# Optimization experiments

Measured on AMD Instinct MI355X. Metric: run time of the kernel, lower is better.

The kernel has to match this reference:

```python
import jax, jax.numpy as jnp
import numpy as np

N_DRUG, N_MICROBE = 1500, 1572
N = N_DRUG + N_MICROBE          # 3072 nodes
F_IN = 1546                     # raw feature dim (fc1: 1546 -> 256)
D0 = 256                        # GCN input dim after fc1
H1 = H2 = 128                   # GCN hidden dims (H1 + H2 = 256)
B = 16384                       # number of (left,right) query pairs


def _sym_norm(A):
    # D^{-1/2} A D^{-1/2} (no self loops), zeros kept for isolated nodes
    deg = A.sum(axis=1)
    d = jnp.where(deg > 0, jax.lax.rsqrt(deg), 0.0)
    return A * d[:, None] * d[None, :]


def _compute_inf(adj, L):
    # dl.compute_inf: L-hop influence = L-th power of sym-normalized adjacency
    An = _sym_norm(adj)
    M = An
    for _ in range(L - 1):
        M = M @ An
    return M


def _gcn_norm(W):
    # GCNConv normalization: add self loops (weight 1), sym-normalize by weighted degree
    Ahat = W + jnp.eye(W.shape[0], dtype=W.dtype)
    deg = Ahat.sum(axis=1)
    d = jnp.where(deg > 0, jax.lax.rsqrt(deg), 0.0)
    return Ahat * d[:, None] * d[None, :]


def _glorot(key, shape):
    return jax.random.normal(key, shape, dtype=jnp.float32) / np.sqrt(shape[0])


def setup_inputs() -> dict:
    key = jax.random.key(0)
    ks = jax.random.split(key, 24)
    u = jax.random.uniform(ks[0], (N, N), dtype=jnp.float32)
    w = jax.random.uniform(ks[1], (N, N), dtype=jnp.float32)
    adj = jnp.where(u < 0.01, w, 0.0)
    adj = jnp.maximum(adj, adj.T)
    X = jax.random.normal(ks[2], (N, F_IN), dtype=jnp.float32)
    left = jax.random.randint(ks[3], (B,), 0, N)
    right = jax.random.randint(ks[4], (B,), 0, N)
    return dict(
        left=left, right=right, X=X, adj=adj, threshold=jnp.float32(1e-4),
        W_fc1=_glorot(ks[5], (F_IN, D0)), b_fc1=jnp.zeros((D0,), jnp.float32),
        Wg1=_glorot(ks[6], (D0, H1)), bg1=jnp.zeros((H1,), jnp.float32),
        Wg2=_glorot(ks[7], (H1, H2)), bg2=jnp.zeros((H2,), jnp.float32),
        Wg3=_glorot(ks[8], (D0, H1)), bg3=jnp.zeros((H1,), jnp.float32),
        Wg4=_glorot(ks[9], (H1, H2)), bg4=jnp.zeros((H2,), jnp.float32),
        Wg5=_glorot(ks[10], (D0, H1)), bg5=jnp.zeros((H1,), jnp.float32),
        Wg6=_glorot(ks[11], (H1, H2)), bg6=jnp.zeros((H2,), jnp.float32),
        cnn_k=jax.random.normal(ks[12], (1, 3, 3, 3), dtype=jnp.float32) * 0.1,
        cnn_b=jnp.zeros((1,), jnp.float32),
        W_a=_glorot(ks[13], (2 * (H1 + H2), 64)), b_a=jnp.zeros((64,), jnp.float32),
        W_b=_glorot(ks[14], (64, 2)), b_b=jnp.zeros((2,), jnp.float32),
    )


def reference(left, right, X, adj, threshold,
              W_fc1, b_fc1, Wg1, bg1, Wg2, bg2, Wg3, bg3, Wg4, bg4,
              Wg5, bg5, Wg6, bg6, cnn_k, cnn_b, W_a, b_a, W_b, b_b):
    X0 = jax.nn.relu(X @ W_fc1 + b_fc1)  # fc1: [N, 1546] -> [N, 256]

    def branch(mask_src, Wa, ba, Wb, bb):
        # dynamically thresholded edges carry the ORIGINAL adj weights
        Wadj = jnp.where(mask_src > threshold, adj, 0.0)
        An = _gcn_norm(Wadj)                       # [N, N]
        e1 = jax.nn.relu(An @ (X0 @ Wa) + ba)      # GCNConv 1
        e2 = jax.nn.relu(An @ (e1 @ Wb) + bb)      # GCNConv 2
        return jnp.concatenate([e1, e2], axis=1)   # [N, 256]

    emb_l2 = branch(_compute_inf(adj, 2), Wg1, bg1, Wg2, bg2)
    emb_l1 = branch(_compute_inf(adj, 1), Wg3, bg3, Wg4, bg4)
    emb_l0 = branch(adj, Wg5, bg5, Wg6, bg6)

    emb = jnp.stack([emb_l0, emb_l1, emb_l2], axis=0)[None]  # [1, 3, N, 256]
    conv = jax.lax.conv_general_dilated(
        emb, cnn_k, window_strides=(1, 1), padding=[(2, 2), (2, 2)],
        rhs_dilation=(2, 2), dimension_numbers=('NCHW', 'OIHW', 'NCHW'))
    emb_all = conv[0, 0] + cnn_b[0]                # [N, 256]

    pair = jnp.concatenate([emb_all[left], emb_all[right]], axis=1)  # [B, 512]
    h = jax.nn.relu(pair @ W_a + b_a)              # dropout is identity at eval
    logits = h @ W_b + b_b                         # [B, 2]
    return logits, emb_all
```

## Files before the change

kernel.cpp:

```cpp
#include <hip/hip_runtime.h>

#define NN 3072
#define FIN 1546
#define KP 1568
#define MAXR 192
#define KSPLIT 7
#define KSLICE 224

typedef __attribute__((ext_vector_type(8))) __bf16 bf16x8;
typedef __attribute__((ext_vector_type(4))) float f32x4;

__global__ __launch_bounds__(256) void csr_k(const float* __restrict__ adj,
                                             int* __restrict__ cols, float* __restrict__ vals,
                                             int* __restrict__ cnt, float* __restrict__ dvec) {
    int i = blockIdx.x * 4 + (threadIdx.x >> 6);
    int lane = threadIdx.x & 63;
    const float* row = adj + (size_t)i * NN;
    float s = 0.f; int count = 0;
    int base = i * MAXR;
    for (int c = 0; c < NN; c += 64) {
        float a = row[c + lane];
        s += a;
        unsigned long long m = __ballot(a != 0.f);
        if (a != 0.f) {
            int pos = count + __popcll(m & ((1ull << lane) - 1ull));
            if (pos < MAXR) { cols[base + pos] = c + lane; vals[base + pos] = a; }
        }
        count += __popcll(m);
    }
    for (int off = 32; off; off >>= 1) s += __shfl_xor(s, off);
    if (lane == 0) {
        cnt[i] = count < MAXR ? count : MAXR;
        dvec[i] = (s > 0.f) ? 1.0f / sqrtf(s) : 0.f;
    }
}

__global__ void xsplit_k(const float* __restrict__ X, __bf16* __restrict__ Xh,
                         __bf16* __restrict__ Xl) {
    int idx = blockIdx.x * 256 + threadIdx.x;
    int i = idx / KP, c = idx - i * KP;
    float x = (c < FIN) ? X[(size_t)i * FIN + c] : 0.f;
    __bf16 h = (__bf16)x;
    Xh[idx] = h;
    Xl[idx] = (__bf16)(x - (float)h);
}

__global__ void wsplit_k(const float* __restrict__ W, __bf16* __restrict__ WhT,
                         __bf16* __restrict__ WlT) {
    int idx = blockIdx.x * 256 + threadIdx.x;
    int c = idx / KP, k = idx - c * KP;
    float x = (k < FIN) ? W[(size_t)k * 256 + c] : 0.f;
    __bf16 h = (__bf16)x;
    WhT[idx] = h;
    WlT[idx] = (__bf16)(x - (float)h);
}

__global__ __launch_bounds__(256) void fc1m_k(const __bf16* __restrict__ Xh,
                                              const __bf16* __restrict__ Xl,
                                              const __bf16* __restrict__ WhT,
                                              const __bf16* __restrict__ WlT,
                                              float* __restrict__ Cpart) {
    int tid = threadIdx.x;
    int w = tid >> 6, lane = tid & 63;
    int m = lane & 15, q = lane >> 4;
    int i0 = blockIdx.x * 64, c0 = blockIdx.y * 64;
    int z = blockIdx.z;
    int k0 = z * KSLICE;
    int rowA = i0 + w * 16 + m;
    const __bf16* xh = Xh + (size_t)rowA * KP + k0 + q * 8;
    const __bf16* xl = Xl + (size_t)rowA * KP + k0 + q * 8;
    const __bf16* bh0 = WhT + (size_t)(c0 + m) * KP + k0 + q * 8;
    const __bf16* bl0 = WlT + (size_t)(c0 + m) * KP + k0 + q * 8;

    f32x4 acc[4];
    #pragma unroll
    for (int ct = 0; ct < 4; ct++)
        #pragma unroll
        for (int r = 0; r < 4; r++) acc[ct][r] = 0.f;

    for (int ks = 0; ks < KSLICE; ks += 32) {
        bf16x8 ah = *(const bf16x8*)(xh + ks);
        bf16x8 al = *(const bf16x8*)(xl + ks);
        #pragma unroll
        for (int ct = 0; ct < 4; ct++) {
            bf16x8 bh = *(const bf16x8*)(bh0 + (size_t)ct * 16 * KP + ks);
            bf16x8 bl = *(const bf16x8*)(bl0 + (size_t)ct * 16 * KP + ks);
            acc[ct] = __builtin_amdgcn_mfma_f32_16x16x32_bf16(ah, bh, acc[ct], 0, 0, 0);
            acc[ct] = __builtin_amdgcn_mfma_f32_16x16x32_bf16(ah, bl, acc[ct], 0, 0, 0);
            acc[ct] = __builtin_amdgcn_mfma_f32_16x16x32_bf16(al, bh, acc[ct], 0, 0, 0);
        }
    }
    float* outp = Cpart + (size_t)z * NN * 256;
    int rowBase = i0 + w * 16 + q * 4;
    #pragma unroll
    for (int ct = 0; ct < 4; ct++) {
        int col = c0 + ct * 16 + m;
        #pragma unroll
        for (int r = 0; r < 4; r++)
            outp[(size_t)(rowBase + r) * 256 + col] = acc[ct][r];
    }
}

__global__ void reduce7_k(const float* __restrict__ Cpart, const float* __restrict__ bias,
                          float* __restrict__ X0) {
    int idx4 = blockIdx.x * 256 + threadIdx.x;
    int c4 = (idx4 & 63) << 2;
    float4 s = ((const float4*)Cpart)[idx4];
    #pragma unroll
    for (int z = 1; z < KSPLIT; z++) {
        float4 t = ((const float4*)(Cpart + (size_t)z * NN * 256))[idx4];
        s.x += t.x; s.y += t.y; s.z += t.z; s.w += t.w;
    }
    float4 b = *(const float4*)&bias[c4];
    s.x = fmaxf(s.x + b.x, 0.f); s.y = fmaxf(s.y + b.y, 0.f);
    s.z = fmaxf(s.z + b.z, 0.f); s.w = fmaxf(s.w + b.w, 0.f);
    ((float4*)X0)[idx4] = s;
}

__global__ __launch_bounds__(256) void maskall_k(const int* __restrict__ cols,
                                                 const float* __restrict__ vals,
                                                 const int* __restrict__ cnt,
                                                 const float* __restrict__ dvec,
                                                 const float* __restrict__ thrp,
                                                 int* __restrict__ mcols,
                                                 float* __restrict__ mvals,
                                                 int* __restrict__ mcnt,
                                                 float* __restrict__ db) {
    __shared__ float ds[NN];
    __shared__ int lcols[MAXR];
    __shared__ float lvals[MAXR];
    __shared__ int lcnt;
    __shared__ float osum;
    int i = blockIdx.x, tid = threadIdx.x, mode = blockIdx.y;
    mcols += (size_t)mode * NN * MAXR;
    mvals += (size_t)mode * NN * MAXR;
    mcnt  += (size_t)mode * NN;
    db    += (size_t)mode * NN;
    int ni = cnt[i], base = i * MAXR;
    float thr = *thrp;
    float di = dvec[i];

    if (mode < 2) {
        if (tid == 0) lcnt = 0;
        __syncthreads();
        float s = 0.f;
        if (tid < ni) {
            int j = cols[base + tid];
            float a = vals[base + tid];
            float m = (mode == 0) ? a : a * di * dvec[j];
            if (m > thr) {
                int p = atomicAdd(&lcnt, 1);
                mcols[base + p] = j;
                mvals[base + p] = a;
                s = a;
            }
        }
        ds[tid] = s; __syncthreads();
        for (int off = 128; off; off >>= 1) {
            if (tid < off) ds[tid] += ds[tid + off];
            __syncthreads();
        }
        if (tid == 0) {
            mcnt[i] = lcnt;
            db[i] = 1.0f / sqrtf(ds[0] + 1.0f);
        }
        return;
    }

    if (tid == 0) { osum = 0.f; lcnt = 0; }
    for (int j = tid; j < NN; j += 256) ds[j] = 0.f;
    __syncthreads();
    for (int t = tid; t < ni; t += 256) {
        int j = cols[base + t];
        float a = vals[base + t];
        lcols[t] = j; lvals[t] = a;
        ds[j] = a * dvec[j] * dvec[j];
    }
    __syncthreads();
    int lane = tid & 63, wv = tid >> 6;
    int sub = lane & 15, dg = lane >> 4;
    for (int o = wv * 4 + dg; o < ni; o += 16) {
        int j = lcols[o];
        int nj = cnt[j], bj = j * MAXR;
        float dot = 0.f;
        for (int t = sub; t < nj; t += 16)
            dot += vals[bj + t] * ds[cols[bj + t]];
        #pragma unroll
        for (int off = 8; off; off >>= 1) dot += __shfl_xor(dot, off);
        if (sub == 0 && di * dvec[j] * dot > thr) {
            int p = atomicAdd(&lcnt, 1);
            mcols[base + p] = j;
            mvals[base + p] = lvals[o];
            atomicAdd(&osum, lvals[o]);
        }
    }
    __syncthreads();
    if (tid == 0) {
        mcnt[i] = lcnt;
        db[i] = 1.0f / sqrtf(osum + 1.0f);
    }
}

__global__ __launch_bounds__(256) void gemm3_k(const float* __restrict__ A, int aplane, int lda,
                                               const float* __restrict__ B0,
                                               const float* __restrict__ B1,
                                               const float* __restrict__ B2,
                                               int K, float* __restrict__ out) {
    __shared__ float Ast[16][68];
    __shared__ float Bs[16][64];
    int tid = threadIdx.x;
    int tx = tid & 15, ty = tid >> 4;
    int i0 = blockIdx.x * 64, c0 = blockIdx.y * 64;
    int z = blockIdx.z;
    const float* Ab = A + (size_t)z * aplane;
    const float* B = (z == 0) ? B0 : (z == 1) ? B1 : B2;
    float* outp = out + (size_t)z * NN * 128;
    int sr = tid >> 4, sk = tid & 15;
    int bk = tid >> 4, bc4 = (tid & 15) << 2;

    float ap[4]; float4 bp;
    #pragma unroll
    for (int u = 0; u < 4; u++) ap[u] = Ab[(size_t)(i0 + sr + u * 16) * lda + sk];
    bp = *(const float4*)&B[(size_t)bk * 128 + c0 + bc4];

    float acc[4][4];
    #pragma unroll
    for (int r = 0; r < 4; r++)
        #pragma unroll
        for (int c = 0; c < 4; c++) acc[r][c] = 0.f;

    for (int kt = 0; kt < K; kt += 16) {
        __syncthreads();
        #pragma unroll
        for (int u = 0; u < 4; u++) Ast[sk][sr + u * 16] = ap[u];
        *(float4*)&Bs[bk][bc4] = bp;
        __syncthreads();
        int kn = kt + 16;
        if (kn < K) {
            #pragma unroll
            for (int u = 0; u < 4; u++) ap[u] = Ab[(size_t)(i0 + sr + u * 16) * lda + kn + sk];
            bp = *(const float4*)&B[(size_t)(kn + bk) * 128 + c0 + bc4];
        }
        #pragma unroll
        for (int kk = 0; kk < 16; kk++) {
            float4 a = *(const float4*)&Ast[kk][ty * 4];
            float4 b = *(const float4*)&Bs[kk][tx * 4];
            const float* av = (const float*)&a;
            const float* bv = (const float*)&b;
            #pragma unroll
            for (int r = 0; r < 4; r++)
                #pragma unroll
                for (int c = 0; c < 4; c++) acc[r][c] += av[r] * bv[c];
        }
    }
    #pragma unroll
    for (int r = 0; r < 4; r++) {
        int row = i0 + ty * 4 + r;
        float4 v = make_float4(acc[r][0], acc[r][1], acc[r][2], acc[r][3]);
        *(float4*)&outp[(size_t)row * 128 + c0 + tx * 4] = v;
    }
}

__global__ __launch_bounds__(256) void spmm3_k(const int* __restrict__ mcols,
                                               const float* __restrict__ mvals,
                                               const int* __restrict__ mcnt,
                                               const float* __restrict__ db,
                                               const float* __restrict__ Xin,
                                               const float* __restrict__ bias0,
                                               const float* __restrict__ bias1,
                                               const float* __restrict__ bias2,
                                               float* __restrict__ outA,
                                               float* __restrict__ embf, int coff) {
    __shared__ float lcoef[MAXR];
    __shared__ int lj[MAXR];
    __shared__ float4 part[8][32];
    int i = blockIdx.x, tid = threadIdx.x, b = blockIdx.y;
    mcols += (size_t)b * NN * MAXR;
    mvals += (size_t)b * NN * MAXR;
    mcnt  += (size_t)b * NN;
    db    += (size_t)b * NN;
    const float* Xb = Xin + (size_t)b * NN * 128;
    const float* bias = (b == 0) ? bias0 : (b == 1) ? bias1 : bias2;
    float dbi = db[i];
    int n = mcnt[i], base = i * MAXR;
    if (tid < n) {
        int j = mcols[base + tid];
        lj[tid] = j;
        lcoef[tid] = mvals[base + tid] * dbi * db[j];
    }
    __syncthreads();
    int g = tid >> 5, c4 = (tid & 31) << 2;
    float4 acc = make_float4(0.f, 0.f, 0.f, 0.f);
    if (g == 0) {
        float4 x = *(const float4*)&Xb[(size_t)i * 128 + c4];
        float d2 = dbi * dbi;
        acc = make_float4(d2 * x.x, d2 * x.y, d2 * x.z, d2 * x.w);
    }
    for (int t = g; t < n; t += 8) {
        float cf = lcoef[t];
        float4 x = *(const float4*)&Xb[(size_t)lj[t] * 128 + c4];
        acc.x += cf * x.x; acc.y += cf * x.y; acc.z += cf * x.z; acc.w += cf * x.w;
    }
    part[g][tid & 31] = acc;
    __syncthreads();
    if (tid < 32) {
        float4 s = part[0][tid];
        #pragma unroll
        for (int gg = 1; gg < 8; gg++) {
            float4 t4 = part[gg][tid];
            s.x += t4.x; s.y += t4.y; s.z += t4.z; s.w += t4.w;
        }
        int cc = tid << 2;
        float4 bv = *(const float4*)&bias[cc];
        s.x = fmaxf(s.x + bv.x, 0.f); s.y = fmaxf(s.y + bv.y, 0.f);
        s.z = fmaxf(s.z + bv.z, 0.f); s.w = fmaxf(s.w + bv.w, 0.f);
        if (outA) *(float4*)&outA[((size_t)b * NN + i) * 128 + cc] = s;
        *(float4*)&embf[((size_t)b * NN + i) * 256 + coff + cc] = s;
    }
}

__global__ __launch_bounds__(256) void conv3f_k(const float* __restrict__ emb,
                                                const float* __restrict__ ck,
                                                const float* __restrict__ cb,
                                                float* __restrict__ outf) {
    __shared__ float rows[3][3][256];
    int n = blockIdx.x, c = threadIdx.x;
    #pragma unroll
    for (int i = 0; i < 3; i++)
        #pragma unroll
        for (int kh = 0; kh < 3; kh++) {
            int nn2 = n + 2 * kh - 2;
            rows[i][kh][c] = (nn2 >= 0 && nn2 < NN) ? emb[((size_t)i * NN + nn2) * 256 + c] : 0.f;
        }
    __syncthreads();
    float s = cb[0];
    #pragma unroll
    for (int i = 0; i < 3; i++)
        #pragma unroll
        for (int kh = 0; kh < 3; kh++)
            #pragma unroll
            for (int kw = 0; kw < 3; kw++) {
                int cc = c + 2 * kw - 2;
                if (cc >= 0 && cc < 256)
                    s += rows[i][kh][cc] * ck[(i * 3 + kh) * 3 + kw];
            }
    outf[(size_t)n * 256 + c] = s;
}

__global__ __launch_bounds__(256) void gemmUV_k(const float* __restrict__ A,
                                                const float* __restrict__ Wa,
                                                float* __restrict__ uvp) {
    __shared__ float Ast[16][68];
    __shared__ float Bs[16][64];
    int tid = threadIdx.x;
    int tx = tid & 15, ty = tid >> 4;
    int i0 = blockIdx.x * 64;
    int half = blockIdx.y;
    int z = blockIdx.z;
    int ks = z * 128;
    const float* Bb = Wa + (half ? 256 * 64 : 0);
    int sr = tid >> 4, sk = tid & 15;
    int bk = tid >> 4, bc4 = (tid & 15) << 2;

    float ap[4]; float4 bp;
    #pragma unroll
    for (int u = 0; u < 4; u++) ap[u] = A[(size_t)(i0 + sr + u * 16) * 256 + ks + sk];
    bp = *(const float4*)&Bb[(size_t)(ks + bk) * 64 + bc4];

    float acc[4][4];
    #pragma unroll
    for (int r = 0; r < 4; r++)
        #pragma unroll
        for (int c = 0; c < 4; c++) acc[r][c] = 0.f;

    for (int kt = ks; kt < ks + 128; kt += 16) {
        __syncthreads();
        #pragma unroll
        for (int u = 0; u < 4; u++) Ast[sk][sr + u * 16] = ap[u];
        *(float4*)&Bs[bk][bc4] = bp;
        __syncthreads();
        int kn = kt + 16;
        if (kn < ks + 128) {
            #pragma unroll
            for (int u = 0; u < 4; u++) ap[u] = A[(size_t)(i0 + sr + u * 16) * 256 + kn + sk];
            bp = *(const float4*)&Bb[(size_t)(kn + bk) * 64 + bc4];
        }
        #pragma unroll
        for (int kk = 0; kk < 16; kk++) {
            float4 a = *(const float4*)&Ast[kk][ty * 4];
            float4 b = *(const float4*)&Bs[kk][tx * 4];
            const float* av = (const float*)&a;
            const float* bv = (const float*)&b;
            #pragma unroll
            for (int r = 0; r < 4; r++)
                #pragma unroll
                for (int c = 0; c < 4; c++) acc[r][c] += av[r] * bv[c];
        }
    }
    float* outp = uvp + (size_t)z * NN * 128;
    #pragma unroll
    for (int r = 0; r < 4; r++) {
        int row = i0 + ty * 4 + r;
        float4 v = make_float4(acc[r][0], acc[r][1], acc[r][2], acc[r][3]);
        *(float4*)&outp[(size_t)row * 128 + half * 64 + tx * 4] = v;
    }
}

__global__ __launch_bounds__(256) void pairuv_k(const int* __restrict__ left,
                                                const int* __restrict__ right,
                                                const float* __restrict__ uvp,
                                                const float* __restrict__ ba,
                                                const float* __restrict__ Wb,
                                                const float* __restrict__ bb,
                                                float* __restrict__ out) {
    int tid = threadIdx.x;
    int w = tid >> 6, c = tid & 63;
    int base = blockIdx.x * 16 + w * 4;
    const float* u0 = uvp;
    const float* u1 = uvp + (size_t)NN * 128;
    float bac = ba[c];
    float w0 = Wb[c * 2], w1 = Wb[c * 2 + 1];
    float b0 = bb[0], b1 = bb[1];
    #pragma unroll
    for (int pp = 0; pp < 4; pp++) {
        int row = base + pp;
        int l = left[row], r = right[row];
        float h = u0[(size_t)l * 128 + c] + u1[(size_t)l * 128 + c]
                + u0[(size_t)r * 128 + 64 + c] + u1[(size_t)r * 128 + 64 + c] + bac;
        h = fmaxf(h, 0.f);
        float s0 = h * w0, s1 = h * w1;
        for (int off = 32; off; off >>= 1) {
            s0 += __shfl_xor(s0, off);
            s1 += __shfl_xor(s1, off);
        }
        if (c == 0) {
            out[row * 2]     = s0 + b0;
            out[row * 2 + 1] = s1 + b1;
        }
    }
}

extern "C" void kernel_launch(void* const* d_in, const int* in_sizes, int n_in,
                              void* d_out, int out_size, void* d_ws, size_t ws_size,
                              hipStream_t stream) {
    const int* left  = (const int*)d_in[0];
    const int* right = (const int*)d_in[1];
    const float* X    = (const float*)d_in[2];
    const float* adj  = (const float*)d_in[3];
    const float* thr  = (const float*)d_in[4];
    const float* Wfc1 = (const float*)d_in[5];
    const float* bfc1 = (const float*)d_in[6];
    const float* Wga[3] = { (const float*)d_in[15], (const float*)d_in[11], (const float*)d_in[7] };
    const float* bga[3] = { (const float*)d_in[16], (const float*)d_in[12], (const float*)d_in[8] };
    const float* Wgb[3] = { (const float*)d_in[17], (const float*)d_in[13], (const float*)d_in[9] };
    const float* bgb[3] = { (const float*)d_in[18], (const float*)d_in[14], (const float*)d_in[10] };
    const float* cnnk = (const float*)d_in[19];
    const float* cnnb = (const float*)d_in[20];
    const float* Wa_  = (const float*)d_in[21];
    const float* ba_  = (const float*)d_in[22];
    const float* Wb_  = (const float*)d_in[23];
    const float* bb_  = (const float*)d_in[24];

    char* p = (char*)d_ws;
    auto take = [&](size_t n) { char* q = p; p += (n + 255) & ~(size_t)255; return q; };
    float* dvec = (float*)take(NN * 4);
    float* db3  = (float*)take((size_t)3 * NN * 4);
    int*   cnt  = (int*)take(NN * 4);
    int*   mcnt3 = (int*)take((size_t)3 * NN * 4);
    int*   cols = (int*)take((size_t)NN * MAXR * 4);
    float* vals = (float*)take((size_t)NN * MAXR * 4);
    int*   mcols3 = (int*)take((size_t)3 * NN * MAXR * 4);
    float* mvals3 = (float*)take((size_t)3 * NN * MAXR * 4);
    float* X0    = (float*)take((size_t)NN * 256 * 4);
    float* XWall = (float*)take((size_t)3 * NN * 128 * 4);
    float* e1all = (float*)take((size_t)3 * NN * 128 * 4);
    float* HW2all= (float*)take((size_t)3 * NN * 128 * 4);
    float* embf  = (float*)take((size_t)3 * NN * 256 * 4);
    __bf16* Xl   = (__bf16*)take((size_t)NN * KP * 2);
    __bf16* WhT  = (__bf16*)take((size_t)256 * KP * 2);
    __bf16* WlT  = (__bf16*)take((size_t)256 * KP * 2);
    __bf16* Xh = (__bf16*)mcols3;
    float* Cpart = XWall;
    float* uvp = embf;

    float* out_logits = (float*)d_out;
    float* out_emb = out_logits + 32768;

    csr_k<<<NN / 4, 256, 0, stream>>>(adj, cols, vals, cnt, dvec);
    xsplit_k<<<NN * KP / 256, 256, 0, stream>>>(X, Xh, Xl);
    wsplit_k<<<256 * KP / 256, 256, 0, stream>>>(Wfc1, WhT, WlT);
    fc1m_k<<<dim3(NN / 64, 4, KSPLIT), 256, 0, stream>>>(Xh, Xl, WhT, WlT, Cpart);
    reduce7_k<<<NN * 64 / 256, 256, 0, stream>>>(Cpart, bfc1, X0);

    maskall_k<<<dim3(NN, 3), 256, 0, stream>>>(cols, vals, cnt, dvec, thr,
                                               mcols3, mvals3, mcnt3, db3);

    gemm3_k<<<dim3(NN / 64, 2, 3), 256, 0, stream>>>(X0, 0, 256, Wga[0], Wga[1], Wga[2], 256, XWall);
    spmm3_k<<<dim3(NN, 3), 256, 0, stream>>>(mcols3, mvals3, mcnt3, db3, XWall,
                                             bga[0], bga[1], bga[2], e1all, embf, 0);
    gemm3_k<<<dim3(NN / 64, 2, 3), 256, 0, stream>>>(e1all, NN * 128, 128, Wgb[0], Wgb[1], Wgb[2], 128, HW2all);
    spmm3_k<<<dim3(NN, 3), 256, 0, stream>>>(mcols3, mvals3, mcnt3, db3, HW2all,
                                             bgb[0], bgb[1], bgb[2], (float*)0, embf, 128);

    conv3f_k<<<NN, 256, 0, stream>>>(embf, cnnk, cnnb, out_emb);
    gemmUV_k<<<dim3(NN / 64, 2, 2), 256, 0, stream>>>(out_emb, Wa_, uvp);
    pairuv_k<<<16384 / 16, 256, 0, stream>>>(left, right, uvp, ba_, Wb_, bb_, out_logits);
}
```

Baseline: 325.2 us.

## Fuse prep kernels and drop split-K in fc1 GEMM with fused bias-ReLU

Merges the CSR build, X split and W split kernels into one launch that dispatches on block index, cutting two launches. The fc1 GEMM drops its 7-way K split and the separate reduction kernel. Each block now has 2 waves covering 32 rows and walks the full K, applying bias and ReLU in the epilogue, so the partial-sum write and re-read go away. The cost is fewer, longer blocks: 384 blocks of 128 threads, each with a serial K loop of 49 steps. That may lower latency hiding compared with the 1344 split-K blocks used before.

```diff
diff --git a/kernel.cpp b/kernel.cpp
--- a/kernel.cpp
+++ b/kernel.cpp
@@ -4,16 +4,43 @@
 #define FIN 1546
 #define KP 1568
 #define MAXR 192
-#define KSPLIT 7
-#define KSLICE 224
+
+#define XSPLIT_BLOCKS (NN * KP / 256)
+#define WSPLIT_BLOCKS (256 * KP / 256)
+#define CSR_BLOCKS (NN / 4)
 
 typedef __attribute__((ext_vector_type(8))) __bf16 bf16x8;
 typedef __attribute__((ext_vector_type(4))) float f32x4;
 
-__global__ __launch_bounds__(256) void csr_k(const float* __restrict__ adj,
-                                             int* __restrict__ cols, float* __restrict__ vals,
-                                             int* __restrict__ cnt, float* __restrict__ dvec) {
-    int i = blockIdx.x * 4 + (threadIdx.x >> 6);
+__global__ __launch_bounds__(256) void prep_k(const float* __restrict__ adj,
+                                              int* __restrict__ cols, float* __restrict__ vals,
+                                              int* __restrict__ cnt, float* __restrict__ dvec,
+                                              const float* __restrict__ X,
+                                              __bf16* __restrict__ Xh, __bf16* __restrict__ Xl,
+                                              const float* __restrict__ W,
+                                              __bf16* __restrict__ WhT, __bf16* __restrict__ WlT) {
+    int bid = blockIdx.x;
+    if (bid < XSPLIT_BLOCKS) {
+        int idx = bid * 256 + threadIdx.x;
+        int i = idx / KP, c = idx - i * KP;
+        float x = (c < FIN) ? X[(size_t)i * FIN + c] : 0.f;
+        __bf16 h = (__bf16)x;
+        Xh[idx] = h;
+        Xl[idx] = (__bf16)(x - (float)h);
+        return;
+    }
+    bid -= XSPLIT_BLOCKS;
+    if (bid < WSPLIT_BLOCKS) {
+        int idx = bid * 256 + threadIdx.x;
+        int c = idx / KP, k = idx - c * KP;
+        float x = (k < FIN) ? W[(size_t)k * 256 + c] : 0.f;
+        __bf16 h = (__bf16)x;
+        WhT[idx] = h;
+        WlT[idx] = (__bf16)(x - (float)h);
+        return;
+    }
+    bid -= WSPLIT_BLOCKS;
+    int i = bid * 4 + (threadIdx.x >> 6);
     int lane = threadIdx.x & 63;
     const float* row = adj + (size_t)i * NN;
     float s = 0.f; int count = 0;
@@ -35,42 +62,21 @@
     }
 }
 
-__global__ void xsplit_k(const float* __restrict__ X, __bf16* __restrict__ Xh,
-                         __bf16* __restrict__ Xl) {
-    int idx = blockIdx.x * 256 + threadIdx.x;
-    int i = idx / KP, c = idx - i * KP;
-    float x = (c < FIN) ? X[(size_t)i * FIN + c] : 0.f;
-    __bf16 h = (__bf16)x;
-    Xh[idx] = h;
-    Xl[idx] = (__bf16)(x - (float)h);
-}
-
-__global__ void wsplit_k(const float* __restrict__ W, __bf16* __restrict__ WhT,
-                         __bf16* __restrict__ WlT) {
-    int idx = blockIdx.x * 256 + threadIdx.x;
-    int c = idx / KP, k = idx - c * KP;
-    float x = (k < FIN) ? W[(size_t)k * 256 + c] : 0.f;
-    __bf16 h = (__bf16)x;
-    WhT[idx] = h;
-    WlT[idx] = (__bf16)(x - (float)h);
-}
-
-__global__ __launch_bounds__(256) void fc1m_k(const __bf16* __restrict__ Xh,
+__global__ __launch_bounds__(128) void fc1m_k(const __bf16* __restrict__ Xh,
                                               const __bf16* __restrict__ Xl,
                                               const __bf16* __restrict__ WhT,
                                               const __bf16* __restrict__ WlT,
-                                              float* __restrict__ Cpart) {
+                                              const float* __restrict__ bias,
+                                              float* __restrict__ X0) {
     int tid = threadIdx.x;
     int w = tid >> 6, lane = tid & 63;
     int m = lane & 15, q = lane >> 4;
-    int i0 = blockIdx.x * 64, c0 = blockIdx.y * 64;
-    int z = blockIdx.z;
-    int k0 = z * KSLICE;
+    int i0 = blockIdx.x * 32, c0 = blockIdx.y * 64;
     int rowA = i0 + w * 16 + m;
-    const __bf16* xh = Xh + (size_t)rowA * KP + k0 + q * 8;
-    const __bf16* xl = Xl + (size_t)rowA * KP + k0 + q * 8;
-    const __bf16* bh0 = WhT + (size_t)(c0 + m) * KP + k0 + q * 8;
-    const __bf16* bl0 = WlT + (size_t)(c0 + m) * KP + k0 + q * 8;
+    const __bf16* xh = Xh + (size_t)rowA * KP + q * 8;
+    const __bf16* xl = Xl + (size_t)rowA * KP + q * 8;
+    const __bf16* bh0 = WhT + (size_t)(c0 + m) * KP + q * 8;
+    const __bf16* bl0 = WlT + (size_t)(c0 + m) * KP + q * 8;
 
     f32x4 acc[4];
     #pragma unroll
@@ -78,7 +84,7 @@
         #pragma unroll
         for (int r = 0; r < 4; r++) acc[ct][r] = 0.f;
 
-    for (int ks = 0; ks < KSLICE; ks += 32) {
+    for (int ks = 0; ks < KP; ks += 32) {
         bf16x8 ah = *(const bf16x8*)(xh + ks);
         bf16x8 al = *(const bf16x8*)(xl + ks);
         #pragma unroll
@@ -90,31 +96,15 @@
             acc[ct] = __builtin_amdgcn_mfma_f32_16x16x32_bf16(al, bh, acc[ct], 0, 0, 0);
         }
     }
-    float* outp = Cpart + (size_t)z * NN * 256;
     int rowBase = i0 + w * 16 + q * 4;
     #pragma unroll
     for (int ct = 0; ct < 4; ct++) {
         int col = c0 + ct * 16 + m;
+        float bc = bias[col];
         #pragma unroll
         for (int r = 0; r < 4; r++)
-            outp[(size_t)(rowBase + r) * 256 + col] = acc[ct][r];
-    }
-}
-
-__global__ void reduce7_k(const float* __restrict__ Cpart, const float* __restrict__ bias,
-                          float* __restrict__ X0) {
-    int idx4 = blockIdx.x * 256 + threadIdx.x;
-    int c4 = (idx4 & 63) << 2;
-    float4 s = ((const float4*)Cpart)[idx4];
-    #pragma unroll
-    for (int z = 1; z < KSPLIT; z++) {
-        float4 t = ((const float4*)(Cpart + (size_t)z * NN * 256))[idx4];
-        s.x += t.x; s.y += t.y; s.z += t.z; s.w += t.w;
-    }
-    float4 b = *(const float4*)&bias[c4];
-    s.x = fmaxf(s.x + b.x, 0.f); s.y = fmaxf(s.y + b.y, 0.f);
-    s.z = fmaxf(s.z + b.z, 0.f); s.w = fmaxf(s.w + b.w, 0.f);
-    ((float4*)X0)[idx4] = s;
+            X0[(size_t)(rowBase + r) * 256 + col] = fmaxf(acc[ct][r] + bc, 0.f);
+    }
 }
 
 __global__ __launch_bounds__(256) void maskall_k(const int* __restrict__ cols,
@@ -480,17 +470,15 @@
     __bf16* WhT  = (__bf16*)take((size_t)256 * KP * 2);
     __bf16* WlT  = (__bf16*)take((size_t)256 * KP * 2);
     __bf16* Xh = (__bf16*)mcols3;
-    float* Cpart = XWall;
     float* uvp = embf;
 
     float* out_logits = (float*)d_out;
     float* out_emb = out_logits + 32768;
 
-    csr_k<<<NN / 4, 256, 0, stream>>>(adj, cols, vals, cnt, dvec);
-    xsplit_k<<<NN * KP / 256, 256, 0, stream>>>(X, Xh, Xl);
-    wsplit_k<<<256 * KP / 256, 256, 0, stream>>>(Wfc1, WhT, WlT);
-    fc1m_k<<<dim3(NN / 64, 4, KSPLIT), 256, 0, stream>>>(Xh, Xl, WhT, WlT, Cpart);
-    reduce7_k<<<NN * 64 / 256, 256, 0, stream>>>(Cpart, bfc1, X0);
+    prep_k<<<XSPLIT_BLOCKS + WSPLIT_BLOCKS + CSR_BLOCKS, 256, 0, stream>>>(
+        adj, cols, vals, cnt, dvec, X, Xh, Xl, Wfc1, WhT, WlT);
+
+    fc1m_k<<<dim3(NN / 32, 4), 128, 0, stream>>>(Xh, Xl, WhT, WlT, bfc1, X0);
 
     maskall_k<<<dim3(NN, 3), 256, 0, stream>>>(cols, vals, cnt, dvec, thr,
                                                mcols3, mvals3, mcnt3, db3);
```

Measured after the change: 398.7 us. 1.23x slower.
